# Kernel tuning notes

Measured on AMD Instinct MI355X. Metric: run time of the kernel, lower is better.

## Reference

```python
import jax, jax.numpy as jnp
import numpy as np

B, T, D = 64, 512, 256   # batch, time, input feat
H = 256                  # LSTM hidden (features)


def setup_inputs() -> dict:
    key = jax.random.key(0)
    ks = jax.random.split(key, 16)
    s = lambda k, shp, fan: jax.random.normal(k, shp, jnp.float32) / np.sqrt(fan)
    return {
        "x":  jax.random.normal(ks[0], (B, T, D), jnp.float32),
        # LSTM params: fused gates order (i, f, g, o)
        "Wi": s(ks[1], (D, 4 * H), D),
        "Wh": s(ks[2], (H, 4 * H), H),
        "b":  jnp.zeros((4 * H,), jnp.float32),
        # single-head attention (head_dim = H)
        "Wq": s(ks[3], (H, H), H), "bq": jnp.zeros((H,), jnp.float32),
        "Wk": s(ks[4], (H, H), H), "bk": jnp.zeros((H,), jnp.float32),
        "Wv": s(ks[5], (H, H), H), "bv": jnp.zeros((H,), jnp.float32),
        "Wo": s(ks[6], (H, H), H), "bo": jnp.zeros((H,), jnp.float32),
        # MLP head
        "W1": s(ks[7], (H, 32), H), "b1": jnp.zeros((32,), jnp.float32),
        "W2": s(ks[8], (32, 3), 32), "b2": jnp.zeros((3,), jnp.float32),
    }


def _lstm_scan(x, Wi, Wh, b):
    # Precompute input-to-hidden projection for all timesteps (batched GEMM)
    xg = jnp.einsum('btd,dg->btg', x, Wi) + b          # [B,T,4H]
    c0 = jnp.zeros((x.shape[0], Wh.shape[0]), x.dtype)
    h0 = jnp.zeros_like(c0)

    def step(carry, xg_t):
        c, h = carry
        g = xg_t + h @ Wh                               # [B,4H]
        i, f, gg, o = jnp.split(g, 4, axis=-1)          # flax gate order i,f,g,o
        c = jax.nn.sigmoid(f) * c + jax.nn.sigmoid(i) * jnp.tanh(gg)
        h = jax.nn.sigmoid(o) * jnp.tanh(c)
        return (c, h), h

    (_, _), hs = jax.lax.scan(step, (c0, h0), jnp.swapaxes(xg, 0, 1))
    return jnp.swapaxes(hs, 0, 1)                       # [B,T,H]


def reference(x, Wi, Wh, b, Wq, bq, Wk, bk, Wv, bv, Wo, bo, W1, b1, W2, b2):
    h = _lstm_scan(x, Wi, Wh, b)                        # [B,T,H]
    # single-head dot-product attention (self-attention)
    q = h @ Wq + bq
    k = h @ Wk + bk
    v = h @ Wv + bv
    scale = 1.0 / np.sqrt(q.shape[-1]).astype(np.float32)
    scores = jnp.einsum('bqd,bkd->bqk', q * scale, k)   # [B,T,T]
    attn = jax.nn.softmax(scores, axis=-1)
    o = jnp.einsum('bqk,bkd->bqd', attn, v)
    o = o @ Wo + bo                                     # output projection
    # head on first timestep
    z = jax.nn.relu(o[:, 0, :] @ W1 + b1)
    return z @ W2 + b2                                  # [B,3]
```

## Files before the change

kernel.cpp:

```cpp
#include <hip/hip_runtime.h>
#include <hip/hip_bf16.h>


typedef __attribute__((ext_vector_type(8))) short short8;
typedef __attribute__((ext_vector_type(4))) float float4v;

__device__ __forceinline__ unsigned short f2bf(float f) {
  unsigned u = __builtin_bit_cast(unsigned, f);
  return (unsigned short)((u + 0x7fffu + ((u >> 16) & 1u)) >> 16);
}
__device__ __forceinline__ float bf2f(unsigned short h) {
  return __builtin_bit_cast(float, ((unsigned)h) << 16);
}
__device__ __forceinline__ float bcl(unsigned u) {
  return __builtin_bit_cast(float, u << 16);
}
__device__ __forceinline__ float bch(unsigned u) {
  return __builtin_bit_cast(float, u & 0xffff0000u);
}
__device__ __forceinline__ float sigm(float x) { return 1.f / (1.f + __expf(-x)); }
__device__ __forceinline__ float tanh_f(float x) { return 1.f - 2.f / (1.f + __expf(2.f * x)); }

__global__ void prep_x(const float* __restrict__ x, unsigned short* __restrict__ xbf) {
  size_t i = ((size_t)blockIdx.x * 256 + threadIdx.x) * 4;
  float4 v = *(const float4*)&x[i];
  unsigned long long pk = (unsigned long long)f2bf(v.x)
                        | ((unsigned long long)f2bf(v.y) << 16)
                        | ((unsigned long long)f2bf(v.z) << 32)
                        | ((unsigned long long)f2bf(v.w) << 48);
  *(unsigned long long*)&xbf[i] = pk;
}

__global__ void prep_wit(const float* __restrict__ Wi, unsigned short* __restrict__ WiT) {
  size_t i = ((size_t)blockIdx.x * 256 + threadIdx.x) * 4;
  float4 v = *(const float4*)&Wi[i];
  int k = (int)(i >> 10), n = (int)(i & 1023);
  WiT[(size_t)(n + 0) * 256 + k] = f2bf(v.x);
  WiT[(size_t)(n + 1) * 256 + k] = f2bf(v.y);
  WiT[(size_t)(n + 2) * 256 + k] = f2bf(v.z);
  WiT[(size_t)(n + 3) * 256 + k] = f2bf(v.w);
}

__global__ void init_hx(unsigned long long* __restrict__ hx) {
  hx[(size_t)blockIdx.x * 256 + threadIdx.x] = 0xffffffff00000000ULL;
}

#define XKP 40
__global__ __launch_bounds__(256) void xg_gemm(const unsigned short* __restrict__ xbf,
                                               const unsigned short* __restrict__ WiT,
                                               const float* __restrict__ bias,
                                               unsigned short* __restrict__ xg) {
  __shared__ unsigned short As[128 * XKP];
  __shared__ unsigned short Bs[128 * XKP];
  const int tid = threadIdx.x;
  const int n0 = blockIdx.x * 128, m0 = blockIdx.y * 128;
  const int wave = tid >> 6, lane = tid & 63, quad = lane >> 4, l16 = lane & 15;
  const int wm = wave >> 1, wn = wave & 1;

  float4v acc[4][4];
#pragma unroll
  for (int i = 0; i < 4; ++i)
#pragma unroll
    for (int j = 0; j < 4; ++j) acc[i][j] = (float4v){0.f, 0.f, 0.f, 0.f};

  const int rr = tid >> 2, c8 = (tid & 3) * 8;
  for (int k0 = 0; k0 < 256; k0 += 32) {
#pragma unroll
    for (int pp = 0; pp < 2; ++pp) {
      int r = pp * 64 + rr;
      *(uint4*)&As[r * XKP + c8] = *(const uint4*)&xbf[(size_t)(m0 + r) * 256 + k0 + c8];
      *(uint4*)&Bs[r * XKP + c8] = *(const uint4*)&WiT[(size_t)(n0 + r) * 256 + k0 + c8];
    }
    __syncthreads();
#pragma unroll
    for (int mt = 0; mt < 4; ++mt) {
      short8 af = *(const short8*)&As[(wm * 64 + mt * 16 + l16) * XKP + quad * 8];
#pragma unroll
      for (int nt = 0; nt < 4; ++nt) {
        short8 bf = *(const short8*)&Bs[(wn * 64 + nt * 16 + l16) * XKP + quad * 8];
        acc[mt][nt] = __builtin_amdgcn_mfma_f32_16x16x32_bf16(af, bf, acc[mt][nt], 0, 0, 0);
      }
    }
    __syncthreads();
  }
#pragma unroll
  for (int nt = 0; nt < 4; ++nt) {
    int col = n0 + wn * 64 + nt * 16 + l16;
    int gate = col >> 8, ggx = (col >> 4) & 15, ul = col & 15;
    float bv = bias[col];
#pragma unroll
    for (int mt = 0; mt < 4; ++mt) {
#pragma unroll
      for (int r = 0; r < 4; ++r) {
        int row = m0 + wm * 64 + mt * 16 + quad * 4 + r;
        int b = row >> 9, t = row & 511;
        xg[(((size_t)ggx * 64 + b) * 512 + t) * 64 + gate * 16 + ul] =
            f2bf(acc[mt][nt][r] + bv);
      }
    }
  }
}

#define KP2 264
__global__ __launch_bounds__(256) void lstm_scan(const float* __restrict__ Wh,
                                                 const unsigned short* __restrict__ xgbuf,
                                                 unsigned short* __restrict__ hout,
                                                 unsigned long long* __restrict__ hx) {
  __shared__ unsigned short WhS[64 * KP2];
  __shared__ unsigned short hA[16 * KP2];
  __shared__ float preS[16 * 68];
  __shared__ float cS[256];
  const int tid = threadIdx.x;
  const int wg = blockIdx.x, bg = wg >> 4, gg = wg & 15;
  const int wave = tid >> 6, lane = tid & 63, quad = lane >> 4, l16 = lane & 15;

  {
    int uu = tid & 15, kh = tid >> 4;
#pragma unroll
    for (int gt = 0; gt < 4; ++gt)
      for (int kb = 0; kb < 16; ++kb) {
        int k = kb * 16 + kh;
        WhS[(gt * 16 + uu) * KP2 + k] = f2bf(Wh[(size_t)k * 1024 + gt * 256 + gg * 16 + uu]);
      }
  }
  for (int i = tid; i < 16 * KP2; i += 256) hA[i] = 0;
  cS[tid] = 0.f;
  __syncthreads();

  const int b_loc = tid >> 4, u_loc = tid & 15;
  const int bgb = bg * 16 + b_loc;
  const int u_glob = gg * 16 + u_loc;
  const int nrow = wave * 16 + l16;
  const unsigned short* xgp0 = xgbuf + ((size_t)(gg * 64 + bgb) * 512) * 64 + u_loc;

  unsigned short xi = xgp0[0], xf = xgp0[16], xG = xgp0[32], xo = xgp0[48];

  for (int t = 0; t < 512; ++t) {
    float4v acc = (float4v){0.f, 0.f, 0.f, 0.f};
#pragma unroll
    for (int kt = 0; kt < 8; ++kt) {
      short8 af = *(const short8*)&hA[l16 * KP2 + kt * 32 + quad * 8];
      short8 bf = *(const short8*)&WhS[nrow * KP2 + kt * 32 + quad * 8];
      acc = __builtin_amdgcn_mfma_f32_16x16x32_bf16(af, bf, acc, 0, 0, 0);
    }
#pragma unroll
    for (int r = 0; r < 4; ++r)
      preS[(quad * 4 + r) * 68 + wave * 16 + l16] = acc[r];

    int tn = (t < 511) ? t + 1 : t;
    const unsigned short* xgn = xgp0 + (size_t)tn * 64;
    unsigned short nxi = xgn[0], nxf = xgn[16], nxG = xgn[32], nxo = xgn[48];
    __syncthreads();

    float gi = preS[b_loc * 68 + 0 * 16 + u_loc] + bf2f(xi);
    float gf = preS[b_loc * 68 + 1 * 16 + u_loc] + bf2f(xf);
    float gG = preS[b_loc * 68 + 2 * 16 + u_loc] + bf2f(xG);
    float go = preS[b_loc * 68 + 3 * 16 + u_loc] + bf2f(xo);
    float c = sigm(gf) * cS[tid] + sigm(gi) * tanh_f(gG);
    cS[tid] = c;
    float h = sigm(go) * tanh_f(c);
    unsigned hb = (unsigned)f2bf(h);
    hA[b_loc * KP2 + u_glob] = (unsigned short)hb;

    const unsigned tg = (unsigned)t;
    unsigned v1 = __shfl_down((int)hb, 1);
    if ((u_loc & 1) == 0) {
      unsigned d0 = hb | (v1 << 16);
      unsigned long long val = (unsigned long long)d0 | ((unsigned long long)tg << 32);
      unsigned long long* dst =
          hx + (((size_t)(t & 1) * 64 + bgb) * 128 + (u_glob >> 1));
      __hip_atomic_store(dst, val, __ATOMIC_RELAXED, __HIP_MEMORY_SCOPE_AGENT);
      *(unsigned*)&hout[((size_t)bgb * 512 + t) * 256 + u_glob] = d0;
    }

    {
      int b2 = tid >> 4, grp = tid & 15;
      if (grp != gg) {
        const unsigned long long* base =
            hx + (((size_t)(t & 1) * 64 + bg * 16 + b2) * 128 + grp * 8);
        unsigned long long w[8];
        int guard = 0;
        bool ok;
        do {
          ok = true;
#pragma unroll
          for (int i = 0; i < 8; ++i) {
            w[i] = __hip_atomic_load(&base[i], __ATOMIC_RELAXED,
                                     __HIP_MEMORY_SCOPE_AGENT);
            ok &= ((unsigned)(w[i] >> 32) == tg);
          }
        } while (!ok && ++guard < (1 << 20));
        int u0 = grp * 16;
#pragma unroll
        for (int i = 0; i < 8; ++i)
          *(unsigned*)&hA[b2 * KP2 + u0 + 2 * i] = (unsigned)w[i];
      }
    }
    xi = nxi; xf = nxf; xG = nxG; xo = nxo;
    __syncthreads();
  }
}

__global__ __launch_bounds__(256) void attn_qu(const unsigned short* __restrict__ hout,
                                               const float* __restrict__ Wq,
                                               const float* __restrict__ bq,
                                               const float* __restrict__ Wk,
                                               const float* __restrict__ bk,
                                               float* __restrict__ us,
                                               float* __restrict__ cbuf) {
  __shared__ float h0S[256], q0S[256], red[256];
  const int b = blockIdx.x, tid = threadIdx.x;
  h0S[tid] = bf2f(hout[(size_t)b * 512 * 256 + tid]);
  __syncthreads();
  float a = 0.f;
  for (int k = 0; k < 256; ++k) a += h0S[k] * Wq[(size_t)k * 256 + tid];
  q0S[tid] = a + bq[tid];
  __syncthreads();
  red[tid] = q0S[tid] * bk[tid];
  __syncthreads();
  for (int s = 128; s > 0; s >>= 1) {
    if (tid < s) red[tid] += red[tid + s];
    __syncthreads();
  }
  if (tid == 0) cbuf[b] = 0.0625f * red[0];
  float acc = 0.f;
  const float* wr = &Wk[(size_t)tid * 256];
  for (int e = 0; e < 256; e += 4) {
    float4 w = *(const float4*)&wr[e];
    acc += w.x * q0S[e] + w.y * q0S[e + 1] + w.z * q0S[e + 2] + w.w * q0S[e + 3];
  }
  us[b * 256 + tid] = 0.0625f * acc;
}

__global__ __launch_bounds__(256) void attn_sm(const unsigned short* __restrict__ hout,
                                               const float* __restrict__ us,
                                               const float* __restrict__ cbuf,
                                               float* __restrict__ hbar) {
  __shared__ float sS[512], red[256], hb4[4][256];
  const int b = blockIdx.x, tid = threadIdx.x, wave = tid >> 6, lane = tid & 63;
  const size_t hb_base = (size_t)b * 512 * 256;
  const float u0 = us[b * 256 + lane * 4 + 0], u1 = us[b * 256 + lane * 4 + 1];
  const float u2 = us[b * 256 + lane * 4 + 2], u3 = us[b * 256 + lane * 4 + 3];
  const float cbv = cbuf[b];
  for (int i = 0; i < 128; ++i) {
    int t = i * 4 + wave;
    unsigned long long hv = *(const unsigned long long*)&hout[hb_base + (size_t)t * 256 + lane * 4];
    unsigned lo = (unsigned)hv, hi = (unsigned)(hv >> 32);
    float p = u0 * bcl(lo) + u1 * bch(lo) + u2 * bcl(hi) + u3 * bch(hi);
    for (int m = 1; m < 64; m <<= 1) p += __shfl_xor(p, m, 64);
    if (lane == 0) sS[t] = p + cbv;
  }
  __syncthreads();
  red[tid] = fmaxf(sS[tid], sS[tid + 256]);
  __syncthreads();
  for (int s = 128; s > 0; s >>= 1) {
    if (tid < s) red[tid] = fmaxf(red[tid], red[tid + s]);
    __syncthreads();
  }
  float mx = red[0];
  __syncthreads();
  float e0 = __expf(sS[tid] - mx), e1 = __expf(sS[tid + 256] - mx);
  sS[tid] = e0; sS[tid + 256] = e1;
  red[tid] = e0 + e1;
  __syncthreads();
  for (int s = 128; s > 0; s >>= 1) {
    if (tid < s) red[tid] += red[tid + s];
    __syncthreads();
  }
  float inv = 1.f / red[0];
  float a0 = 0.f, a1 = 0.f, a2 = 0.f, a3 = 0.f;
  const int d0 = lane * 4;
  for (int i = 0; i < 128; ++i) {
    int t = wave * 128 + i;
    float w = sS[t];
    unsigned long long hv = *(const unsigned long long*)&hout[hb_base + (size_t)t * 256 + d0];
    unsigned lo = (unsigned)hv, hi = (unsigned)(hv >> 32);
    a0 += w * bcl(lo); a1 += w * bch(lo); a2 += w * bcl(hi); a3 += w * bch(hi);
  }
  hb4[wave][d0] = a0; hb4[wave][d0 + 1] = a1; hb4[wave][d0 + 2] = a2; hb4[wave][d0 + 3] = a3;
  __syncthreads();
  hbar[b * 256 + tid] = (hb4[0][tid] + hb4[1][tid] + hb4[2][tid] + hb4[3][tid]) * inv;
}

__global__ __launch_bounds__(256) void head_k(const float* __restrict__ hbar,
                                              const float* __restrict__ Wv, const float* __restrict__ bv,
                                              const float* __restrict__ Wo, const float* __restrict__ bo,
                                              const float* __restrict__ W1, const float* __restrict__ b1,
                                              const float* __restrict__ W2, const float* __restrict__ b2,
                                              float* __restrict__ out) {
  __shared__ float hS[256], oS[256], o1S[256], zS[32];
  const int b = blockIdx.x, tid = threadIdx.x;
  hS[tid] = hbar[b * 256 + tid];
  __syncthreads();
  float a = 0.f;
  for (int k = 0; k < 256; ++k) a += hS[k] * Wv[(size_t)k * 256 + tid];
  oS[tid] = a + bv[tid];
  __syncthreads();
  a = 0.f;
  for (int k = 0; k < 256; ++k) a += oS[k] * Wo[(size_t)k * 256 + tid];
  o1S[tid] = a + bo[tid];
  __syncthreads();
  if (tid < 32) {
    a = 0.f;
    for (int k = 0; k < 256; ++k) a += o1S[k] * W1[k * 32 + tid];
    zS[tid] = fmaxf(a + b1[tid], 0.f);
  }
  __syncthreads();
  if (tid < 3) {
    a = 0.f;
    for (int j = 0; j < 32; ++j) a += zS[j] * W2[j * 3 + tid];
    out[b * 3 + tid] = a + b2[tid];
  }
}

extern "C" void kernel_launch(void* const* d_in, const int* in_sizes, int n_in,
                              void* d_out, int out_size, void* d_ws, size_t ws_size,
                              hipStream_t stream) {
  const float* x  = (const float*)d_in[0];
  const float* Wi = (const float*)d_in[1];
  const float* Wh = (const float*)d_in[2];
  const float* bG = (const float*)d_in[3];
  const float* Wq = (const float*)d_in[4];
  const float* bq = (const float*)d_in[5];
  const float* Wk = (const float*)d_in[6];
  const float* bk = (const float*)d_in[7];
  const float* Wv = (const float*)d_in[8];
  const float* bv = (const float*)d_in[9];
  const float* Wo = (const float*)d_in[10];
  const float* bo = (const float*)d_in[11];
  const float* W1 = (const float*)d_in[12];
  const float* b1 = (const float*)d_in[13];
  const float* W2 = (const float*)d_in[14];
  const float* b2 = (const float*)d_in[15];
  float* out = (float*)d_out;
  char* ws = (char*)d_ws;

  unsigned short* xg    = (unsigned short*)(ws);
  unsigned short* hout  = (unsigned short*)(ws + 67108864);
  unsigned short* xbf   = (unsigned short*)(ws + 83886080);
  unsigned short* WiT   = (unsigned short*)(ws + 100663296);
  unsigned long long* hx = (unsigned long long*)(ws + 101187584);
  float*          us    = (float*)(ws + 101318656);
  float*          cbuf  = (float*)(ws + 101384192);
  float*          hbar  = (float*)(ws + 101385216);

  prep_x<<<dim3(8192), dim3(256), 0, stream>>>(x, xbf);
  prep_wit<<<dim3(256), dim3(256), 0, stream>>>(Wi, WiT);
  init_hx<<<dim3(64), dim3(256), 0, stream>>>(hx);
  xg_gemm<<<dim3(8, 256), dim3(256), 0, stream>>>(xbf, WiT, bG, xg);
  lstm_scan<<<dim3(64), dim3(256), 0, stream>>>(Wh, xg, hout, hx);
  attn_qu<<<dim3(64), dim3(256), 0, stream>>>(hout, Wq, bq, Wk, bk, us, cbuf);
  attn_sm<<<dim3(64), dim3(256), 0, stream>>>(hout, us, cbuf, hbar);
  head_k<<<dim3(64), dim3(256), 0, stream>>>(hbar, Wv, bv, Wo, bo, W1, b1, W2, b2, out);
}
```

Baseline: 1.406 ms.

## Restructure LSTM scan into 8 blocks holding Wh fragments in registers

The recurrent scan now runs 8 workgroups of 512 threads instead of 64 of 256. Each pair of blocks splits the hidden units of a 16-batch group, so each block exchanges h with only one peer instead of fifteen. Wh is pre-transposed to bf16 and kept entirely in registers as MFMA fragments. The local half of the matmul is issued before waiting on the peer's half, and h is double-buffered in LDS with gate math done straight from the accumulators. The xg layout changes to time-contiguous per unit. This trades a much smaller grid and heavy register use for fewer cross-block sync points per step.

```diff
diff --git a/kernel.cpp b/kernel.cpp
--- a/kernel.cpp
+++ b/kernel.cpp
@@ -18,8 +18,12 @@
 __device__ __forceinline__ float bch(unsigned u) {
   return __builtin_bit_cast(float, u & 0xffff0000u);
 }
-__device__ __forceinline__ float sigm(float x) { return 1.f / (1.f + __expf(-x)); }
-__device__ __forceinline__ float tanh_f(float x) { return 1.f - 2.f / (1.f + __expf(2.f * x)); }
+__device__ __forceinline__ float sigm(float x) {
+  return __builtin_amdgcn_rcpf(1.f + __expf(-x));
+}
+__device__ __forceinline__ float tanh_f(float x) {
+  return 1.f - 2.f * __builtin_amdgcn_rcpf(1.f + __expf(2.f * x));
+}
 
 __global__ void prep_x(const float* __restrict__ x, unsigned short* __restrict__ xbf) {
   size_t i = ((size_t)blockIdx.x * 256 + threadIdx.x) * 4;
@@ -31,14 +35,14 @@
   *(unsigned long long*)&xbf[i] = pk;
 }
 
-__global__ void prep_wit(const float* __restrict__ Wi, unsigned short* __restrict__ WiT) {
+__global__ void prep_wit(const float* __restrict__ W, unsigned short* __restrict__ WT) {
   size_t i = ((size_t)blockIdx.x * 256 + threadIdx.x) * 4;
-  float4 v = *(const float4*)&Wi[i];
+  float4 v = *(const float4*)&W[i];
   int k = (int)(i >> 10), n = (int)(i & 1023);
-  WiT[(size_t)(n + 0) * 256 + k] = f2bf(v.x);
-  WiT[(size_t)(n + 1) * 256 + k] = f2bf(v.y);
-  WiT[(size_t)(n + 2) * 256 + k] = f2bf(v.z);
-  WiT[(size_t)(n + 3) * 256 + k] = f2bf(v.w);
+  WT[(size_t)(n + 0) * 256 + k] = f2bf(v.x);
+  WT[(size_t)(n + 1) * 256 + k] = f2bf(v.y);
+  WT[(size_t)(n + 2) * 256 + k] = f2bf(v.z);
+  WT[(size_t)(n + 3) * 256 + k] = f2bf(v.w);
 }
 
 __global__ void init_hx(unsigned long long* __restrict__ hx) {
@@ -86,7 +90,7 @@
 #pragma unroll
   for (int nt = 0; nt < 4; ++nt) {
     int col = n0 + wn * 64 + nt * 16 + l16;
-    int gate = col >> 8, ggx = (col >> 4) & 15, ul = col & 15;
+    int gate = col >> 8, u = col & 255;
     float bv = bias[col];
 #pragma unroll
     for (int mt = 0; mt < 4; ++mt) {
@@ -94,109 +98,133 @@
       for (int r = 0; r < 4; ++r) {
         int row = m0 + wm * 64 + mt * 16 + quad * 4 + r;
         int b = row >> 9, t = row & 511;
-        xg[(((size_t)ggx * 64 + b) * 512 + t) * 64 + gate * 16 + ul] =
-            f2bf(acc[mt][nt][r] + bv);
+        xg[(((size_t)gate * 256 + u) * 64 + b) * 512 + t] = f2bf(acc[mt][nt][r] + bv);
       }
     }
   }
 }
 
-#define KP2 264
-__global__ __launch_bounds__(256) void lstm_scan(const float* __restrict__ Wh,
-                                                 const unsigned short* __restrict__ xgbuf,
-                                                 unsigned short* __restrict__ hout,
-                                                 unsigned long long* __restrict__ hx) {
-  __shared__ unsigned short WhS[64 * KP2];
-  __shared__ unsigned short hA[16 * KP2];
-  __shared__ float preS[16 * 68];
-  __shared__ float cS[256];
+#define HAP 264
+__global__ __launch_bounds__(512, 2) void lstm_scan(
+    const unsigned short* __restrict__ WhT,
+    const unsigned short* __restrict__ xgbuf,
+    unsigned short* __restrict__ hout,
+    unsigned long long* __restrict__ hx) {
+  __shared__ unsigned short hA[2 * 16 * HAP];
   const int tid = threadIdx.x;
-  const int wg = blockIdx.x, bg = wg >> 4, gg = wg & 15;
+  const int wg = blockIdx.x;
+  const int bg = wg >> 1, ug = wg & 1;
   const int wave = tid >> 6, lane = tid & 63, quad = lane >> 4, l16 = lane & 15;
-
-  {
-    int uu = tid & 15, kh = tid >> 4;
-#pragma unroll
-    for (int gt = 0; gt < 4; ++gt)
-      for (int kb = 0; kb < 16; ++kb) {
-        int k = kb * 16 + kh;
-        WhS[(gt * 16 + uu) * KP2 + k] = f2bf(Wh[(size_t)k * 1024 + gt * 256 + gg * 16 + uu]);
+  const int u_loc = wave * 16 + l16;
+  const int u_glob = ug * 128 + u_loc;
+
+  short8 fr[4][8];
+#pragma unroll
+  for (int g = 0; g < 4; ++g) {
+    const unsigned short* src = WhT + ((size_t)(g * 256 + u_glob)) * 256 + quad * 8;
+#pragma unroll
+    for (int p = 0; p < 8; ++p) {
+      int kt = (ug * 4 + p) & 7;
+      fr[g][p] = *(const short8*)&src[kt * 32];
+    }
+  }
+  for (int i = tid; i < 2 * 16 * HAP; i += 512) hA[i] = 0;
+
+  const int b0g = bg * 16 + quad * 4;
+  const unsigned short* xgp = xgbuf + ((size_t)u_glob * 64 + b0g) * 512;
+  float c[4] = {0.f, 0.f, 0.f, 0.f};
+  unsigned short cx[4][4], nx[4][4];
+#pragma unroll
+  for (int g = 0; g < 4; ++g)
+#pragma unroll
+    for (int r = 0; r < 4; ++r) cx[g][r] = xgp[(size_t)g * 8388608 + r * 512];
+
+  __syncthreads();
+
+  for (int t = 0; t < 512; ++t) {
+    unsigned short* buf = &hA[(t & 1) * 16 * HAP];
+    float4v acc[4];
+#pragma unroll
+    for (int g = 0; g < 4; ++g) acc[g] = (float4v){0.f, 0.f, 0.f, 0.f};
+
+#pragma unroll
+    for (int p = 0; p < 4; ++p) {
+      int colk = (ug * 128 + p * 32) & 255;
+      short8 a = *(const short8*)&buf[l16 * HAP + colk + quad * 8];
+#pragma unroll
+      for (int g = 0; g < 4; ++g)
+        acc[g] = __builtin_amdgcn_mfma_f32_16x16x32_bf16(a, fr[g][p], acc[g], 0, 0, 0);
+    }
+
+    int tn = (t < 511) ? t + 1 : t;
+#pragma unroll
+    for (int g = 0; g < 4; ++g)
+#pragma unroll
+      for (int r = 0; r < 4; ++r) nx[g][r] = xgp[(size_t)g * 8388608 + r * 512 + tn];
+
+    if (t > 0) {
+      const unsigned tg = (unsigned)(t - 1);
+      const unsigned long long* pb =
+          hx + (size_t)((t & 1) ^ 1) * 8192 + (size_t)(1 - ug) * 4096 + (size_t)bg * 1024;
+      unsigned long long w0, w1;
+      int guard = 0;
+      bool ok;
+      do {
+        w0 = __hip_atomic_load(&pb[tid], __ATOMIC_RELAXED, __HIP_MEMORY_SCOPE_AGENT);
+        w1 = __hip_atomic_load(&pb[tid + 512], __ATOMIC_RELAXED, __HIP_MEMORY_SCOPE_AGENT);
+        ok = ((unsigned)(w0 >> 32) == tg) & ((unsigned)(w1 >> 32) == tg);
+      } while (!ok && ++guard < (1 << 20));
+      *(unsigned*)&buf[(tid >> 6) * HAP + (1 - ug) * 128 + 2 * (tid & 63)] = (unsigned)w0;
+      *(unsigned*)&buf[((tid >> 6) + 8) * HAP + (1 - ug) * 128 + 2 * (tid & 63)] = (unsigned)w1;
+    }
+    __syncthreads();
+
+#pragma unroll
+    for (int p = 4; p < 8; ++p) {
+      int colk = (ug * 128 + p * 32) & 255;
+      short8 a = *(const short8*)&buf[l16 * HAP + colk + quad * 8];
+#pragma unroll
+      for (int g = 0; g < 4; ++g)
+        acc[g] = __builtin_amdgcn_mfma_f32_16x16x32_bf16(a, fr[g][p], acc[g], 0, 0, 0);
+    }
+
+    unsigned hw_[4];
+#pragma unroll
+    for (int r = 0; r < 4; ++r) {
+      float gi = acc[0][r] + bf2f(cx[0][r]);
+      float gf = acc[1][r] + bf2f(cx[1][r]);
+      float gG = acc[2][r] + bf2f(cx[2][r]);
+      float go = acc[3][r] + bf2f(cx[3][r]);
+      float cc = sigm(gf) * c[r] + sigm(gi) * tanh_f(gG);
+      c[r] = cc;
+      hw_[r] = (unsigned)f2bf(sigm(go) * tanh_f(cc));
+    }
+
+    unsigned p_[4];
+#pragma unroll
+    for (int r = 0; r < 4; ++r)
+      p_[r] = hw_[r] | ((unsigned)__shfl_down((int)hw_[r], 1) << 16);
+    if ((l16 & 1) == 0) {
+      const int j = u_loc >> 1;
+#pragma unroll
+      for (int r = 0; r < 4; ++r) {
+        const int bglob = b0g + r;
+        unsigned long long val =
+            (unsigned long long)p_[r] | ((unsigned long long)(unsigned)t << 32);
+        __hip_atomic_store(
+            hx + (size_t)(t & 1) * 8192 + (size_t)ug * 4096 + (size_t)bglob * 64 + j,
+            val, __ATOMIC_RELAXED, __HIP_MEMORY_SCOPE_AGENT);
+        *(unsigned*)&hout[((size_t)bglob * 512 + t) * 256 + u_glob] = p_[r];
       }
-  }
-  for (int i = tid; i < 16 * KP2; i += 256) hA[i] = 0;
-  cS[tid] = 0.f;
-  __syncthreads();
-
-  const int b_loc = tid >> 4, u_loc = tid & 15;
-  const int bgb = bg * 16 + b_loc;
-  const int u_glob = gg * 16 + u_loc;
-  const int nrow = wave * 16 + l16;
-  const unsigned short* xgp0 = xgbuf + ((size_t)(gg * 64 + bgb) * 512) * 64 + u_loc;
-
-  unsigned short xi = xgp0[0], xf = xgp0[16], xG = xgp0[32], xo = xgp0[48];
-
-  for (int t = 0; t < 512; ++t) {
-    float4v acc = (float4v){0.f, 0.f, 0.f, 0.f};
-#pragma unroll
-    for (int kt = 0; kt < 8; ++kt) {
-      short8 af = *(const short8*)&hA[l16 * KP2 + kt * 32 + quad * 8];
-      short8 bf = *(const short8*)&WhS[nrow * KP2 + kt * 32 + quad * 8];
-      acc = __builtin_amdgcn_mfma_f32_16x16x32_bf16(af, bf, acc, 0, 0, 0);
-    }
-#pragma unroll
-    for (int r = 0; r < 4; ++r)
-      preS[(quad * 4 + r) * 68 + wave * 16 + l16] = acc[r];
-
-    int tn = (t < 511) ? t + 1 : t;
-    const unsigned short* xgn = xgp0 + (size_t)tn * 64;
-    unsigned short nxi = xgn[0], nxf = xgn[16], nxG = xgn[32], nxo = xgn[48];
-    __syncthreads();
-
-    float gi = preS[b_loc * 68 + 0 * 16 + u_loc] + bf2f(xi);
-    float gf = preS[b_loc * 68 + 1 * 16 + u_loc] + bf2f(xf);
-    float gG = preS[b_loc * 68 + 2 * 16 + u_loc] + bf2f(xG);
-    float go = preS[b_loc * 68 + 3 * 16 + u_loc] + bf2f(xo);
-    float c = sigm(gf) * cS[tid] + sigm(gi) * tanh_f(gG);
-    cS[tid] = c;
-    float h = sigm(go) * tanh_f(c);
-    unsigned hb = (unsigned)f2bf(h);
-    hA[b_loc * KP2 + u_glob] = (unsigned short)hb;
-
-    const unsigned tg = (unsigned)t;
-    unsigned v1 = __shfl_down((int)hb, 1);
-    if ((u_loc & 1) == 0) {
-      unsigned d0 = hb | (v1 << 16);
-      unsigned long long val = (unsigned long long)d0 | ((unsigned long long)tg << 32);
-      unsigned long long* dst =
-          hx + (((size_t)(t & 1) * 64 + bgb) * 128 + (u_glob >> 1));
-      __hip_atomic_store(dst, val, __ATOMIC_RELAXED, __HIP_MEMORY_SCOPE_AGENT);
-      *(unsigned*)&hout[((size_t)bgb * 512 + t) * 256 + u_glob] = d0;
-    }
-
-    {
-      int b2 = tid >> 4, grp = tid & 15;
-      if (grp != gg) {
-        const unsigned long long* base =
-            hx + (((size_t)(t & 1) * 64 + bg * 16 + b2) * 128 + grp * 8);
-        unsigned long long w[8];
-        int guard = 0;
-        bool ok;
-        do {
-          ok = true;
-#pragma unroll
-          for (int i = 0; i < 8; ++i) {
-            w[i] = __hip_atomic_load(&base[i], __ATOMIC_RELAXED,
-                                     __HIP_MEMORY_SCOPE_AGENT);
-            ok &= ((unsigned)(w[i] >> 32) == tg);
-          }
-        } while (!ok && ++guard < (1 << 20));
-        int u0 = grp * 16;
-#pragma unroll
-        for (int i = 0; i < 8; ++i)
-          *(unsigned*)&hA[b2 * KP2 + u0 + 2 * i] = (unsigned)w[i];
-      }
-    }
-    xi = nxi; xf = nxf; xG = nxG; xo = nxo;
+    }
+    unsigned short* nbuf = &hA[((t + 1) & 1) * 16 * HAP];
+#pragma unroll
+    for (int r = 0; r < 4; ++r) nbuf[(quad * 4 + r) * HAP + u_glob] = (unsigned short)hw_[r];
+
+#pragma unroll
+    for (int g = 0; g < 4; ++g)
+#pragma unroll
+      for (int r = 0; r < 4; ++r) cx[g][r] = nx[g][r];
     __syncthreads();
   }
 }
@@ -338,6 +366,7 @@
   unsigned short* xg    = (unsigned short*)(ws);
   unsigned short* hout  = (unsigned short*)(ws + 67108864);
   unsigned short* xbf   = (unsigned short*)(ws + 83886080);
+  unsigned short* WhT   = (unsigned short*)(ws + 83886080);
   unsigned short* WiT   = (unsigned short*)(ws + 100663296);
   unsigned long long* hx = (unsigned long long*)(ws + 101187584);
   float*          us    = (float*)(ws + 101318656);
@@ -348,7 +377,8 @@
   prep_wit<<<dim3(256), dim3(256), 0, stream>>>(Wi, WiT);
   init_hx<<<dim3(64), dim3(256), 0, stream>>>(hx);
   xg_gemm<<<dim3(8, 256), dim3(256), 0, stream>>>(xbf, WiT, bG, xg);
-  lstm_scan<<<dim3(64), dim3(256), 0, stream>>>(Wh, xg, hout, hx);
+  prep_wit<<<dim3(256), dim3(256), 0, stream>>>(Wh, WhT);
+  lstm_scan<<<dim3(8), dim3(512), 0, stream>>>(WhT, xg, hout, hx);
   attn_qu<<<dim3(64), dim3(256), 0, stream>>>(hout, Wq, bq, Wk, bk, us, cbuf);
   attn_sm<<<dim3(64), dim3(256), 0, stream>>>(hout, us, cbuf, hbar);
   head_k<<<dim3(64), dim3(256), 0, stream>>>(hbar, Wv, bv, Wo, bo, W1, b1, W2, b2, out);
```

After: 3.340 ms. +137.5%, slower.
